# Kernel optimization log

Hardware: AMD Instinct MI355X
Metric: run time of the kernel (lower is better)

## Reference

```python
import jax, jax.numpy as jnp
import numpy as np

D_MODEL = 1024
NHEAD = 16
HEAD_DIM = D_MODEL // NHEAD  # 64
AXIS_DIM = HEAD_DIM // 4     # 16
DFF = 4096
EPS = 1e-5
BASE = 10000.0
B, S = 4, 2048


def setup_inputs() -> dict:
    key = jax.random.key(0)
    ks = jax.random.split(key, 10)
    def xavier(k, shape):
        fan_in, fan_out = shape[1], shape[0]
        limit = np.sqrt(6.0 / (fan_in + fan_out))
        return jax.random.uniform(k, shape, jnp.float32, -limit, limit)
    return {
        "src": jax.random.normal(ks[0], (B, S, D_MODEL), jnp.float32),
        "positions": jax.random.normal(ks[1], (B, S, 4), jnp.float32),
        "w_qkv": xavier(ks[2], (3 * D_MODEL, D_MODEL)),
        "w_out": xavier(ks[3], (D_MODEL, D_MODEL)),
        "norm1_w": jnp.ones((D_MODEL,), jnp.float32),
        "norm2_w": jnp.ones((D_MODEL,), jnp.float32),
        "w1": xavier(ks[4], (DFF, D_MODEL)),
        "w2": xavier(ks[5], (D_MODEL, DFF)),
        "w3": xavier(ks[6], (DFF, D_MODEL)),
        "axis_scale": jnp.ones((4,), jnp.float32),
    }


def _rmsnorm(x, w, eps=EPS):
    return x * jax.lax.rsqrt(jnp.mean(x * x, axis=-1, keepdims=True) + eps) * w


def _rope_rotate(x, cos, sin):
    # x: (B,H,S,HEAD_DIM); cos/sin: (B,1,S,4,AXIS_DIM//2)
    b, h, s, _ = x.shape
    xr = x.reshape(b, h, s, 4, AXIS_DIM // 2, 2)  # 4 axis chunks, interleaved pairs
    e, o = xr[..., 0], xr[..., 1]
    re = e * cos - o * sin
    ro = o * cos + e * sin
    return jnp.stack([re, ro], axis=-1).reshape(b, h, s, HEAD_DIM)


def reference(src, positions, w_qkv, w_out, norm1_w, norm2_w, w1, w2, w3, axis_scale):
    b, s, _ = src.shape
    x = src
    x_norm = _rmsnorm(x, norm1_w)
    qkv = x_norm @ w_qkv.T  # (B,S,3*D)
    qkv = qkv.reshape(b, s, 3, NHEAD, HEAD_DIM).transpose(2, 0, 3, 1, 4)
    q, k, v = qkv[0], qkv[1], qkv[2]  # (B,H,S,Dh)

    # 4D RoPE: same inv_freq per axis (base^{-idx/axis_dim})
    inv_freq = BASE ** (-(jnp.arange(0, AXIS_DIM, 2, dtype=jnp.float32) / AXIS_DIM))  # (8,)
    coord = positions * axis_scale  # (B,S,4)
    angles = coord[..., None] * inv_freq  # (B,S,4,8)
    cos = jnp.cos(angles)[:, None]  # (B,1,S,4,8)
    sin = jnp.sin(angles)[:, None]
    q = _rope_rotate(q, cos, sin)
    k = _rope_rotate(k, cos, sin)

    scale = 1.0 / jnp.sqrt(jnp.float32(HEAD_DIM))
    scores = jnp.einsum("bhqd,bhkd->bhqk", q, k) * scale
    attn = jax.nn.softmax(scores, axis=-1)
    attn_out = jnp.einsum("bhqk,bhkd->bhqd", attn, v)
    attn_out = attn_out.transpose(0, 2, 1, 3).reshape(b, s, D_MODEL)
    x = x + attn_out @ w_out.T

    x_norm = _rmsnorm(x, norm2_w)
    ff = (jax.nn.silu(x_norm @ w1.T) * (x_norm @ w3.T)) @ w2.T
    return x + ff
```

## Files before the change

kernel.cpp:

```cpp
#include <hip/hip_runtime.h>

typedef unsigned short u16;
typedef __attribute__((ext_vector_type(4))) unsigned short u16x4;
typedef __attribute__((ext_vector_type(8))) short bf16x8;
typedef __attribute__((ext_vector_type(4))) float f32x4;
typedef __attribute__((ext_vector_type(16))) float f32x16;

__device__ __forceinline__ float bf2f(u16 u) {
  union { unsigned i; float f; } v; v.i = ((unsigned)u) << 16; return v.f;
}
__device__ __forceinline__ u16 f2bf(float f) {
  union { float f; unsigned i; } v; v.f = f;
  unsigned r = v.i + 0x7fffu + ((v.i >> 16) & 1u);
  return (u16)(r >> 16);
}
__device__ __forceinline__ void gl_lds16(const u16* g, u16* l) {
  __builtin_amdgcn_global_load_lds((const __attribute__((address_space(1))) unsigned*)g,
                                   (__attribute__((address_space(3))) unsigned*)l, 16, 0, 0);
}
__device__ __forceinline__ f32x16 mfma32(bf16x8 a, bf16x8 b, f32x16 c) {
  return __builtin_amdgcn_mfma_f32_32x32x16_bf16(a, b, c, 0, 0, 0);
}

__global__ __launch_bounds__(256) void k_cvt5(const float* __restrict__ s0, const float* __restrict__ s1,
                                              const float* __restrict__ s2, const float* __restrict__ s3,
                                              const float* __restrict__ s4,
                                              u16* __restrict__ d0, u16* __restrict__ d1,
                                              u16* __restrict__ d2, u16* __restrict__ d3,
                                              u16* __restrict__ d4) {
  int b = blockIdx.x;
  const float* S; u16* D; int off;
  if (b < 1536)      { S = s0; D = d0; off = b; }
  else if (b < 2048) { S = s1; D = d1; off = b - 1536; }
  else if (b < 4096) { S = s2; D = d2; off = b - 2048; }
  else if (b < 6144) { S = s3; D = d3; off = b - 4096; }
  else               { S = s4; D = d4; off = b - 6144; }
  int i = (off * 256 + threadIdx.x) * 8;
  f32x4 a = *(const f32x4*)(S + i), c = *(const f32x4*)(S + i + 4);
  bf16x8 r;
  r[0] = (short)f2bf(a.x); r[1] = (short)f2bf(a.y); r[2] = (short)f2bf(a.z); r[3] = (short)f2bf(a.w);
  r[4] = (short)f2bf(c.x); r[5] = (short)f2bf(c.y); r[6] = (short)f2bf(c.z); r[7] = (short)f2bf(c.w);
  *(bf16x8*)(D + i) = r;
}

__global__ __launch_bounds__(256) void k_rmsnorm(const void* __restrict__ X,
                                                 const float* __restrict__ W,
                                                 u16* __restrict__ Y, int x_ext) {
  const int tok = blockIdx.x, t = threadIdx.x;
  float x0, x1, x2, x3;
  if (x_ext) {
    f32x4 xv = ((const f32x4*)X)[tok * 256 + t];
    x0 = xv.x; x1 = xv.y; x2 = xv.z; x3 = xv.w;
  } else {
    u16x4 xv = ((const u16x4*)X)[tok * 256 + t];
    x0 = bf2f(xv.x); x1 = bf2f(xv.y); x2 = bf2f(xv.z); x3 = bf2f(xv.w);
  }
  float ss = x0 * x0 + x1 * x1 + x2 * x2 + x3 * x3;
#pragma unroll
  for (int m = 32; m; m >>= 1) ss += __shfl_xor(ss, m);
  __shared__ float red[4];
  if ((t & 63) == 0) red[t >> 6] = ss;
  __syncthreads();
  float inv = rsqrtf((red[0] + red[1] + red[2] + red[3]) * (1.f / 1024.f) + 1e-5f);
  f32x4 wv = ((const f32x4*)W)[t];
  u16x4 o;
  o.x = f2bf(x0 * inv * wv.x);
  o.y = f2bf(x1 * inv * wv.y);
  o.z = f2bf(x2 * inv * wv.z);
  o.w = f2bf(x3 * inv * wv.w);
  ((u16x4*)(Y + (size_t)tok * 1024))[t] = o;
}

template <int EPI, int OUTF32>
__global__ __launch_bounds__(256, 2) void k_gemm(const u16* __restrict__ A,
                                                 const u16* __restrict__ W,
                                                 const void* R, void* C,
                                                 int M, int N, int K, int r_ext) {
  __shared__ u16 sA[128 * 64];
  __shared__ u16 sB[128 * 64];
  const int t = threadIdx.x;
  const int wid = t >> 6, lane = t & 63, quad = lane >> 4, l16 = lane & 15;
  const int wm = wid >> 1, wn = wid & 1;
  const size_t m0 = (size_t)blockIdx.y * 128, n0 = (size_t)blockIdx.x * 128;
  f32x4 acc[4][4] = {};
  const int srow = wid * 32 + (lane >> 3);
  const int schunk = (lane & 7) ^ ((lane >> 3) & 7);
  const u16* Ag = A + (m0 + srow) * K + schunk * 8;
  const u16* Wg = W + (n0 + srow) * (size_t)K + schunk * 8;
  const int xk = l16 & 7;
  for (int k0 = 0; k0 < K; k0 += 64) {
#pragma unroll
    for (int i = 0; i < 4; ++i) {
      gl_lds16(Ag + (size_t)i * 8 * K + k0, sA + wid * 2048 + i * 512 + lane * 8);
      gl_lds16(Wg + (size_t)i * 8 * K + k0, sB + wid * 2048 + i * 512 + lane * 8);
    }
    __syncthreads();
#pragma unroll
    for (int ks = 0; ks < 2; ++ks) {
      const int slot = ((ks * 4 + quad) ^ xk) * 8;
      bf16x8 a[4], b[4];
#pragma unroll
      for (int mt = 0; mt < 4; ++mt)
        a[mt] = *(const bf16x8*)(sA + (wm * 64 + mt * 16 + l16) * 64 + slot);
#pragma unroll
      for (int nt = 0; nt < 4; ++nt)
        b[nt] = *(const bf16x8*)(sB + (wn * 64 + nt * 16 + l16) * 64 + slot);
#pragma unroll
      for (int mt = 0; mt < 4; ++mt)
#pragma unroll
        for (int nt = 0; nt < 4; ++nt)
          acc[mt][nt] = __builtin_amdgcn_mfma_f32_16x16x32_bf16(a[mt], b[nt], acc[mt][nt], 0, 0, 0);
    }
    __syncthreads();
  }
#pragma unroll
  for (int mt = 0; mt < 4; ++mt) {
#pragma unroll
    for (int nt = 0; nt < 4; ++nt) {
      size_t row = m0 + wm * 64 + mt * 16 + quad * 4;
      size_t col = n0 + wn * 64 + nt * 16 + l16;
#pragma unroll
      for (int r = 0; r < 4; ++r) {
        float v = acc[mt][nt][r];
        size_t idx = (row + r) * N + col;
        if (EPI == 1) v += r_ext ? ((const float*)R)[idx] : bf2f(((const u16*)R)[idx]);
        if (OUTF32) ((float*)C)[idx] = v;
        else ((u16*)C)[idx] = f2bf(v);
      }
    }
  }
}

__global__ __launch_bounds__(256, 2) void k_ffn(const u16* __restrict__ A,
                                                const u16* __restrict__ W1,
                                                const u16* __restrict__ W3,
                                                u16* __restrict__ C,
                                                int M, int N, int K) {
  __shared__ u16 sA[128 * 64];
  __shared__ u16 sB1[128 * 64];
  __shared__ u16 sB3[128 * 64];
  const int t = threadIdx.x;
  const int wid = t >> 6, lane = t & 63, quad = lane >> 4, l16 = lane & 15;
  const int wm = wid >> 1, wn = wid & 1;
  const size_t m0 = (size_t)blockIdx.y * 128, n0 = (size_t)blockIdx.x * 128;
  f32x4 acc1[4][4] = {};
  f32x4 acc3[4][4] = {};
  const int srow = wid * 32 + (lane >> 3);
  const int schunk = (lane & 7) ^ ((lane >> 3) & 7);
  const u16* Ag = A + (m0 + srow) * K + schunk * 8;
  const u16* W1g = W1 + (n0 + srow) * (size_t)K + schunk * 8;
  const u16* W3g = W3 + (n0 + srow) * (size_t)K + schunk * 8;
  const int xk = l16 & 7;
  for (int k0 = 0; k0 < K; k0 += 64) {
#pragma unroll
    for (int i = 0; i < 4; ++i) {
      gl_lds16(Ag + (size_t)i * 8 * K + k0, sA + wid * 2048 + i * 512 + lane * 8);
      gl_lds16(W1g + (size_t)i * 8 * K + k0, sB1 + wid * 2048 + i * 512 + lane * 8);
      gl_lds16(W3g + (size_t)i * 8 * K + k0, sB3 + wid * 2048 + i * 512 + lane * 8);
    }
    __syncthreads();
#pragma unroll
    for (int ks = 0; ks < 2; ++ks) {
      const int slot = ((ks * 4 + quad) ^ xk) * 8;
      bf16x8 a[4], b1[4], b3[4];
#pragma unroll
      for (int mt = 0; mt < 4; ++mt)
        a[mt] = *(const bf16x8*)(sA + (wm * 64 + mt * 16 + l16) * 64 + slot);
#pragma unroll
      for (int nt = 0; nt < 4; ++nt) {
        b1[nt] = *(const bf16x8*)(sB1 + (wn * 64 + nt * 16 + l16) * 64 + slot);
        b3[nt] = *(const bf16x8*)(sB3 + (wn * 64 + nt * 16 + l16) * 64 + slot);
      }
#pragma unroll
      for (int mt = 0; mt < 4; ++mt)
#pragma unroll
        for (int nt = 0; nt < 4; ++nt) {
          acc1[mt][nt] = __builtin_amdgcn_mfma_f32_16x16x32_bf16(a[mt], b1[nt], acc1[mt][nt], 0, 0, 0);
          acc3[mt][nt] = __builtin_amdgcn_mfma_f32_16x16x32_bf16(a[mt], b3[nt], acc3[mt][nt], 0, 0, 0);
        }
    }
    __syncthreads();
  }
#pragma unroll
  for (int mt = 0; mt < 4; ++mt) {
#pragma unroll
    for (int nt = 0; nt < 4; ++nt) {
      size_t row = m0 + wm * 64 + mt * 16 + quad * 4;
      size_t col = n0 + wn * 64 + nt * 16 + l16;
#pragma unroll
      for (int r = 0; r < 4; ++r) {
        float v1 = acc1[mt][nt][r];
        float v3 = acc3[mt][nt][r];
        float h = v1 / (1.f + __expf(-v1)) * v3;
        C[(row + r) * N + col] = f2bf(h);
      }
    }
  }
}

#define SCL 0.18033688011112042f

__global__ __launch_bounds__(256) void k_rope(const u16* __restrict__ QKV,
                                              const float* __restrict__ POS,
                                              const float* __restrict__ ASC,
                                              u16* __restrict__ Qr, u16* __restrict__ Kr,
                                              u16* __restrict__ Vt) {
  const int bh = blockIdx.x, b = bh >> 4, h = bh & 15;
  const int s0 = blockIdx.y * 128;
  const int t = threadIdx.x;
  const int pr = t & 31, a = pr >> 3, f = pr & 7, srow = t >> 5;
  const float asc = ASC[a];
  const float invf = exp2f(-(float)f * (13.28771237954945f / 8.f));
  for (int pass = 0; pass < 16; ++pass) {
    int s = s0 + pass * 8 + srow;
    float ang = POS[((size_t)b * 2048 + s) * 4 + a] * asc * invf;
    float sn, cs;
    sincosf(ang, &sn, &cs);
    size_t ib = ((size_t)b * 2048 + s) * 3072 + h * 64 + a * 16 + f * 2;
    size_t ob = ((size_t)bh * 2048 + s) * 64 + a * 16 + f * 2;
    unsigned qw = *(const unsigned*)(QKV + ib);
    float e = bf2f((u16)(qw & 0xffff)), o = bf2f((u16)(qw >> 16));
    *(unsigned*)(Qr + ob) =
        (unsigned)f2bf((e * cs - o * sn) * SCL) | ((unsigned)f2bf((o * cs + e * sn) * SCL) << 16);
    unsigned kw = *(const unsigned*)(QKV + ib + 1024);
    e = bf2f((u16)(kw & 0xffff));
    o = bf2f((u16)(kw >> 16));
    *(unsigned*)(Kr + ob) = (unsigned)f2bf(e * cs - o * sn) | ((unsigned)f2bf(o * cs + e * sn) << 16);
  }
  __shared__ u16 vt[64 * 130];
#pragma unroll
  for (int it = 0; it < 32; ++it) {
    int idx = it * 256 + t, sl = idx >> 6, d = idx & 63;
    vt[d * 130 + sl] = QKV[((size_t)b * 2048 + s0 + sl) * 3072 + 2048 + h * 64 + d];
  }
  __syncthreads();
#pragma unroll
  for (int it = 0; it < 32; ++it) {
    int idx = it * 256 + t, d = idx >> 7, sl = idx & 127;
    Vt[((size_t)bh * 64 + d) * 2048 + s0 + sl] = vt[d * 130 + sl];
  }
}

__global__ __launch_bounds__(256, 3) void k_attn(const u16* __restrict__ Qr,
                                                 const u16* __restrict__ Kr,
                                                 const u16* __restrict__ Vt,
                                                 u16* __restrict__ O) {
  __shared__ u16 sK[2][4096];
  __shared__ u16 sV[2][4096];
  const int t = threadIdx.x, wid = t >> 6, lane = t & 63;
  const int il = lane & 31, hh = lane >> 5;
  const int bh = blockIdx.x;
  const int q0 = blockIdx.y * 128 + wid * 32;
  const size_t base = (size_t)bh * 2048 * 64;

  bf16x8 qf[4];
#pragma unroll
  for (int c = 0; c < 4; ++c)
    qf[c] = *(const bf16x8*)(Qr + base + (size_t)(q0 + il) * 64 + c * 16 + hh * 8);

  bf16x8 ones;
#pragma unroll
  for (int i = 0; i < 8; ++i) ones[i] = (short)0x3F80;

  const f32x16 ZERO = {};
  f32x16 oa[2] = {ZERO, ZERO};
  f32x16 ol = ZERO;

  const u16* Kb = Kr + base;
  const u16* Vb = Vt + base;
  const int cc = t & 7, r0 = t >> 3;
  {
    bf16x8 k0 = *(const bf16x8*)(Kb + (size_t)r0 * 64 + cc * 8);
    bf16x8 k1 = *(const bf16x8*)(Kb + (size_t)(r0 + 32) * 64 + cc * 8);
    bf16x8 v0 = *(const bf16x8*)(Vb + (size_t)r0 * 2048 + cc * 8);
    bf16x8 v1 = *(const bf16x8*)(Vb + (size_t)(r0 + 32) * 2048 + cc * 8);
    *(bf16x8*)(sK[0] + (cc * 64 + (r0 ^ cc)) * 8) = k0;
    *(bf16x8*)(sK[0] + (cc * 64 + ((r0 + 32) ^ cc)) * 8) = k1;
    *(bf16x8*)(sV[0] + (cc * 64 + (r0 ^ cc)) * 8) = v0;
    *(bf16x8*)(sV[0] + (cc * 64 + ((r0 + 32) ^ cc)) * 8) = v1;
  }
  __syncthreads();

  for (int it = 0; it < 32; ++it) {
    const u16* kb = sK[it & 1];
    const u16* vb = sV[it & 1];
    bf16x8 nk0, nk1, nv0, nv1;
    const int last = (it == 31);
    if (!last) {
      int kv = (it + 1) * 64;
      nk0 = *(const bf16x8*)(Kb + (size_t)(kv + r0) * 64 + cc * 8);
      nk1 = *(const bf16x8*)(Kb + (size_t)(kv + r0 + 32) * 64 + cc * 8);
      nv0 = *(const bf16x8*)(Vb + (size_t)r0 * 2048 + kv + cc * 8);
      nv1 = *(const bf16x8*)(Vb + (size_t)(r0 + 32) * 2048 + kv + cc * 8);
    }
    f32x16 sacc[2];
    __builtin_amdgcn_s_setprio(1);
#pragma unroll
    for (int kt = 0; kt < 2; ++kt) {
#pragma unroll
      for (int c = 0; c < 4; ++c) {
        int ch = c * 2 + hh;
        bf16x8 kf = *(const bf16x8*)(kb + (ch * 64 + ((kt * 32 + il) ^ ch)) * 8);
        sacc[kt] = (c == 0) ? mfma32(kf, qf[0], ZERO) : mfma32(kf, qf[c], sacc[kt]);
      }
    }
    __builtin_amdgcn_s_setprio(0);
    bf16x8 pa[4];
#pragma unroll
    for (int kt = 0; kt < 2; ++kt) {
      float p[16];
#pragma unroll
      for (int r = 0; r < 16; ++r) p[r] = exp2f(sacc[kt][r]);
      unsigned w[8];
#pragma unroll
      for (int i = 0; i < 8; ++i)
        asm("v_cvt_pk_bf16_f32 %0, %1, %2" : "=v"(w[i]) : "v"(p[2 * i]), "v"(p[2 * i + 1]));
      asm("v_permlane32_swap_b32 %0, %1" : "+v"(w[0]), "+v"(w[2]));
      asm("v_permlane32_swap_b32 %0, %1" : "+v"(w[1]), "+v"(w[3]));
      asm("v_permlane32_swap_b32 %0, %1" : "+v"(w[4]), "+v"(w[6]));
      asm("v_permlane32_swap_b32 %0, %1" : "+v"(w[5]), "+v"(w[7]));
      union { unsigned u[4]; bf16x8 v; } f0, f1;
      f0.u[0] = w[0]; f0.u[1] = w[1]; f0.u[2] = w[2]; f0.u[3] = w[3];
      f1.u[0] = w[4]; f1.u[1] = w[5]; f1.u[2] = w[6]; f1.u[3] = w[7];
      pa[kt * 2] = f0.v;
      pa[kt * 2 + 1] = f1.v;
    }
    __builtin_amdgcn_s_setprio(1);
#pragma unroll
    for (int ks = 0; ks < 4; ++ks) {
      int sc = ks * 2 + hh;
      ol = mfma32(ones, pa[ks], ol);
#pragma unroll
      for (int dt = 0; dt < 2; ++dt) {
        bf16x8 vf = *(const bf16x8*)(vb + (sc * 64 + ((dt * 32 + il) ^ sc)) * 8);
        oa[dt] = mfma32(vf, pa[ks], oa[dt]);
      }
    }
    __builtin_amdgcn_s_setprio(0);
    if (!last) {
      u16* kn = sK[(it + 1) & 1];
      u16* vn = sV[(it + 1) & 1];
      *(bf16x8*)(kn + (cc * 64 + (r0 ^ cc)) * 8) = nk0;
      *(bf16x8*)(kn + (cc * 64 + ((r0 + 32) ^ cc)) * 8) = nk1;
      *(bf16x8*)(vn + (cc * 64 + (r0 ^ cc)) * 8) = nv0;
      *(bf16x8*)(vn + (cc * 64 + ((r0 + 32) ^ cc)) * 8) = nv1;
    }
    __syncthreads();
  }
  const int b = bh >> 4, hd = bh & 15;
  {
    float inv = 1.f / ol[0];
    int q = q0 + il;
#pragma unroll
    for (int dt = 0; dt < 2; ++dt) {
#pragma unroll
      for (int g = 0; g < 4; ++g) {
        u16x4 pk;
        pk.x = f2bf(oa[dt][4 * g + 0] * inv);
        pk.y = f2bf(oa[dt][4 * g + 1] * inv);
        pk.z = f2bf(oa[dt][4 * g + 2] * inv);
        pk.w = f2bf(oa[dt][4 * g + 3] * inv);
        *(u16x4*)(O + ((size_t)b * 2048 + q) * 1024 + hd * 64 + dt * 32 + 8 * g + 4 * hh) = pk;
      }
    }
  }
}

extern "C" void kernel_launch(void* const* d_in, const int* in_sizes, int n_in,
                              void* d_out, int out_size, void* d_ws, size_t ws_size,
                              hipStream_t stream) {
  const float* src    = (const float*)d_in[0];
  const float* pos    = (const float*)d_in[1];
  const float* w_qkv  = (const float*)d_in[2];
  const float* w_out  = (const float*)d_in[3];
  const float* n1w    = (const float*)d_in[4];
  const float* n2w    = (const float*)d_in[5];
  const float* w1     = (const float*)d_in[6];
  const float* w2     = (const float*)d_in[7];
  const float* w3     = (const float*)d_in[8];
  const float* ascale = (const float*)d_in[9];
  char* ws = (char*)d_ws;
  u16* xn  = (u16*)(ws);
  u16* qkv = (u16*)(ws + ((size_t)16 << 20));
  u16* Qr  = (u16*)(ws);
  u16* Kr  = (u16*)(ws + ((size_t)64 << 20));
  u16* Vt  = (u16*)(ws + ((size_t)80 << 20));
  u16* att = (u16*)(ws + ((size_t)16 << 20));
  u16* x   = (u16*)(ws + ((size_t)80 << 20));
  u16* xn2 = (u16*)(ws);
  u16* h1  = (u16*)(ws + ((size_t)16 << 20));
  u16* bqkv = (u16*)(ws + ((size_t)96 << 20));
  u16* bout = (u16*)(ws + ((size_t)102 << 20));
  u16* b1   = (u16*)(ws + ((size_t)104 << 20));
  u16* b3   = (u16*)(ws + ((size_t)112 << 20));
  u16* b2   = (u16*)(ws + ((size_t)120 << 20));

  k_cvt5<<<8192, 256, 0, stream>>>(w_qkv, w_out, w1, w3, w2, bqkv, bout, b1, b3, b2);

  k_rmsnorm<<<8192, 256, 0, stream>>>(src, n1w, xn, 1);
  k_gemm<0, 0><<<dim3(24, 64), 256, 0, stream>>>(xn, bqkv, nullptr, qkv, 8192, 3072, 1024, 0);
  k_rope<<<dim3(64, 16), 256, 0, stream>>>(qkv, pos, ascale, Qr, Kr, Vt);
  k_attn<<<dim3(64, 16), 256, 0, stream>>>(Qr, Kr, Vt, att);
  k_gemm<1, 0><<<dim3(8, 64), 256, 0, stream>>>(att, bout, src, x, 8192, 1024, 1024, 1);
  k_rmsnorm<<<8192, 256, 0, stream>>>(x, n2w, xn2, 0);
  k_ffn<<<dim3(32, 64), 256, 0, stream>>>(xn2, b1, b3, h1, 8192, 4096, 1024);
  k_gemm<1, 1><<<dim3(8, 64), 256, 0, stream>>>(h1, b2, x, d_out, 8192, 1024, 4096, 0);
}
```

Baseline: 621.9 us.

## Double-buffer GEMM and FFN LDS tiles with BK=32 prefetch pipeline

```diff
diff --git a/kernel.cpp b/kernel.cpp
--- a/kernel.cpp
+++ b/kernel.cpp
@@ -72,46 +72,56 @@
 }
 
 template <int EPI, int OUTF32>
-__global__ __launch_bounds__(256, 2) void k_gemm(const u16* __restrict__ A,
+__global__ __launch_bounds__(256, 3) void k_gemm(const u16* __restrict__ A,
                                                  const u16* __restrict__ W,
                                                  const void* R, void* C,
                                                  int M, int N, int K, int r_ext) {
-  __shared__ u16 sA[128 * 64];
-  __shared__ u16 sB[128 * 64];
+  __shared__ u16 sA[2][4096];
+  __shared__ u16 sB[2][4096];
   const int t = threadIdx.x;
   const int wid = t >> 6, lane = t & 63, quad = lane >> 4, l16 = lane & 15;
   const int wm = wid >> 1, wn = wid & 1;
   const size_t m0 = (size_t)blockIdx.y * 128, n0 = (size_t)blockIdx.x * 128;
   f32x4 acc[4][4] = {};
-  const int srow = wid * 32 + (lane >> 3);
-  const int schunk = (lane & 7) ^ ((lane >> 3) & 7);
+  const int srow = t >> 2, schunk = (t & 3) ^ ((t >> 3) & 3);
   const u16* Ag = A + (m0 + srow) * K + schunk * 8;
   const u16* Wg = W + (n0 + srow) * (size_t)K + schunk * 8;
-  const int xk = l16 & 7;
-  for (int k0 = 0; k0 < K; k0 += 64) {
-#pragma unroll
-    for (int i = 0; i < 4; ++i) {
-      gl_lds16(Ag + (size_t)i * 8 * K + k0, sA + wid * 2048 + i * 512 + lane * 8);
-      gl_lds16(Wg + (size_t)i * 8 * K + k0, sB + wid * 2048 + i * 512 + lane * 8);
-    }
-    __syncthreads();
-#pragma unroll
-    for (int ks = 0; ks < 2; ++ks) {
-      const int slot = ((ks * 4 + quad) ^ xk) * 8;
-      bf16x8 a[4], b[4];
-#pragma unroll
-      for (int mt = 0; mt < 4; ++mt)
-        a[mt] = *(const bf16x8*)(sA + (wm * 64 + mt * 16 + l16) * 64 + slot);
+  const int csw = (quad ^ ((l16 >> 1) & 3)) * 8;
+  const int dofs = wid * 512 + lane * 8;
+  gl_lds16(Ag, &sA[0][0] + dofs);
+  gl_lds16(Ag + (size_t)64 * K, &sA[0][0] + dofs + 2048);
+  gl_lds16(Wg, &sB[0][0] + dofs);
+  gl_lds16(Wg + (size_t)64 * K, &sB[0][0] + dofs + 2048);
+  asm volatile("s_waitcnt vmcnt(0)" ::: "memory");
+  __builtin_amdgcn_s_barrier();
+  const int ntile = K >> 5;
+  for (int kt = 0; kt < ntile; ++kt) {
+    const int cur = kt & 1, nxt = cur ^ 1;
+    if (kt + 1 < ntile) {
+      const int k0 = (kt + 1) << 5;
+      gl_lds16(Ag + k0, &sA[nxt][0] + dofs);
+      gl_lds16(Ag + (size_t)64 * K + k0, &sA[nxt][0] + dofs + 2048);
+      gl_lds16(Wg + k0, &sB[nxt][0] + dofs);
+      gl_lds16(Wg + (size_t)64 * K + k0, &sB[nxt][0] + dofs + 2048);
+    }
+    bf16x8 a[4], b[4];
+#pragma unroll
+    for (int mt = 0; mt < 4; ++mt)
+      a[mt] = *(const bf16x8*)(&sA[cur][0] + (wm * 64 + mt * 16 + l16) * 32 + csw);
+#pragma unroll
+    for (int nt = 0; nt < 4; ++nt)
+      b[nt] = *(const bf16x8*)(&sB[cur][0] + (wn * 64 + nt * 16 + l16) * 32 + csw);
+    asm volatile("s_waitcnt lgkmcnt(0)" ::: "memory");
+    __builtin_amdgcn_sched_barrier(0);
+    __builtin_amdgcn_s_setprio(1);
+#pragma unroll
+    for (int mt = 0; mt < 4; ++mt)
 #pragma unroll
       for (int nt = 0; nt < 4; ++nt)
-        b[nt] = *(const bf16x8*)(sB + (wn * 64 + nt * 16 + l16) * 64 + slot);
-#pragma unroll
-      for (int mt = 0; mt < 4; ++mt)
-#pragma unroll
-        for (int nt = 0; nt < 4; ++nt)
-          acc[mt][nt] = __builtin_amdgcn_mfma_f32_16x16x32_bf16(a[mt], b[nt], acc[mt][nt], 0, 0, 0);
-    }
-    __syncthreads();
+        acc[mt][nt] = __builtin_amdgcn_mfma_f32_16x16x32_bf16(a[mt], b[nt], acc[mt][nt], 0, 0, 0);
+    __builtin_amdgcn_s_setprio(0);
+    asm volatile("s_waitcnt vmcnt(0)" ::: "memory");
+    __builtin_amdgcn_s_barrier();
   }
 #pragma unroll
   for (int mt = 0; mt < 4; ++mt) {
@@ -136,50 +146,63 @@
                                                 const u16* __restrict__ W3,
                                                 u16* __restrict__ C,
                                                 int M, int N, int K) {
-  __shared__ u16 sA[128 * 64];
-  __shared__ u16 sB1[128 * 64];
-  __shared__ u16 sB3[128 * 64];
+  __shared__ u16 sA[2][4096];
+  __shared__ u16 sB1[2][4096];
+  __shared__ u16 sB3[2][4096];
   const int t = threadIdx.x;
   const int wid = t >> 6, lane = t & 63, quad = lane >> 4, l16 = lane & 15;
   const int wm = wid >> 1, wn = wid & 1;
   const size_t m0 = (size_t)blockIdx.y * 128, n0 = (size_t)blockIdx.x * 128;
   f32x4 acc1[4][4] = {};
   f32x4 acc3[4][4] = {};
-  const int srow = wid * 32 + (lane >> 3);
-  const int schunk = (lane & 7) ^ ((lane >> 3) & 7);
+  const int srow = t >> 2, schunk = (t & 3) ^ ((t >> 3) & 3);
   const u16* Ag = A + (m0 + srow) * K + schunk * 8;
   const u16* W1g = W1 + (n0 + srow) * (size_t)K + schunk * 8;
   const u16* W3g = W3 + (n0 + srow) * (size_t)K + schunk * 8;
-  const int xk = l16 & 7;
-  for (int k0 = 0; k0 < K; k0 += 64) {
-#pragma unroll
-    for (int i = 0; i < 4; ++i) {
-      gl_lds16(Ag + (size_t)i * 8 * K + k0, sA + wid * 2048 + i * 512 + lane * 8);
-      gl_lds16(W1g + (size_t)i * 8 * K + k0, sB1 + wid * 2048 + i * 512 + lane * 8);
-      gl_lds16(W3g + (size_t)i * 8 * K + k0, sB3 + wid * 2048 + i * 512 + lane * 8);
-    }
-    __syncthreads();
-#pragma unroll
-    for (int ks = 0; ks < 2; ++ks) {
-      const int slot = ((ks * 4 + quad) ^ xk) * 8;
-      bf16x8 a[4], b1[4], b3[4];
-#pragma unroll
-      for (int mt = 0; mt < 4; ++mt)
-        a[mt] = *(const bf16x8*)(sA + (wm * 64 + mt * 16 + l16) * 64 + slot);
+  const int csw = (quad ^ ((l16 >> 1) & 3)) * 8;
+  const int dofs = wid * 512 + lane * 8;
+  gl_lds16(Ag, &sA[0][0] + dofs);
+  gl_lds16(Ag + (size_t)64 * K, &sA[0][0] + dofs + 2048);
+  gl_lds16(W1g, &sB1[0][0] + dofs);
+  gl_lds16(W1g + (size_t)64 * K, &sB1[0][0] + dofs + 2048);
+  gl_lds16(W3g, &sB3[0][0] + dofs);
+  gl_lds16(W3g + (size_t)64 * K, &sB3[0][0] + dofs + 2048);
+  asm volatile("s_waitcnt vmcnt(0)" ::: "memory");
+  __builtin_amdgcn_s_barrier();
+  const int ntile = K >> 5;
+  for (int kt = 0; kt < ntile; ++kt) {
+    const int cur = kt & 1, nxt = cur ^ 1;
+    if (kt + 1 < ntile) {
+      const int k0 = (kt + 1) << 5;
+      gl_lds16(Ag + k0, &sA[nxt][0] + dofs);
+      gl_lds16(Ag + (size_t)64 * K + k0, &sA[nxt][0] + dofs + 2048);
+      gl_lds16(W1g + k0, &sB1[nxt][0] + dofs);
+      gl_lds16(W1g + (size_t)64 * K + k0, &sB1[nxt][0] + dofs + 2048);
+      gl_lds16(W3g + k0, &sB3[nxt][0] + dofs);
+      gl_lds16(W3g + (size_t)64 * K + k0, &sB3[nxt][0] + dofs + 2048);
+    }
+    bf16x8 a[4], b1[4], b3[4];
+#pragma unroll
+    for (int mt = 0; mt < 4; ++mt)
+      a[mt] = *(const bf16x8*)(&sA[cur][0] + (wm * 64 + mt * 16 + l16) * 32 + csw);
+#pragma unroll
+    for (int nt = 0; nt < 4; ++nt) {
+      b1[nt] = *(const bf16x8*)(&sB1[cur][0] + (wn * 64 + nt * 16 + l16) * 32 + csw);
+      b3[nt] = *(const bf16x8*)(&sB3[cur][0] + (wn * 64 + nt * 16 + l16) * 32 + csw);
+    }
+    asm volatile("s_waitcnt lgkmcnt(0)" ::: "memory");
+    __builtin_amdgcn_sched_barrier(0);
+    __builtin_amdgcn_s_setprio(1);
+#pragma unroll
+    for (int mt = 0; mt < 4; ++mt)
 #pragma unroll
       for (int nt = 0; nt < 4; ++nt) {
-        b1[nt] = *(const bf16x8*)(sB1 + (wn * 64 + nt * 16 + l16) * 64 + slot);
-        b3[nt] = *(const bf16x8*)(sB3 + (wn * 64 + nt * 16 + l16) * 64 + slot);
-      }
-#pragma unroll
-      for (int mt = 0; mt < 4; ++mt)
-#pragma unroll
-        for (int nt = 0; nt < 4; ++nt) {
-          acc1[mt][nt] = __builtin_amdgcn_mfma_f32_16x16x32_bf16(a[mt], b1[nt], acc1[mt][nt], 0, 0, 0);
-          acc3[mt][nt] = __builtin_amdgcn_mfma_f32_16x16x32_bf16(a[mt], b3[nt], acc3[mt][nt], 0, 0, 0);
-        }
-    }
-    __syncthreads();
+        acc1[mt][nt] = __builtin_amdgcn_mfma_f32_16x16x32_bf16(a[mt], b1[nt], acc1[mt][nt], 0, 0, 0);
+        acc3[mt][nt] = __builtin_amdgcn_mfma_f32_16x16x32_bf16(a[mt], b3[nt], acc3[mt][nt], 0, 0, 0);
+      }
+    __builtin_amdgcn_s_setprio(0);
+    asm volatile("s_waitcnt vmcnt(0)" ::: "memory");
+    __builtin_amdgcn_s_barrier();
   }
 #pragma unroll
   for (int mt = 0; mt < 4; ++mt) {
```

Measured after the change: 675.3 us. 1.09x slower.
